# Kernel optimization log

Hardware: AMD Instinct MI355X
Metric: run time of the kernel (lower is better)

## Reference

```python
import jax, jax.numpy as jnp
import numpy as np

B, L, D, H = 2, 2048, 1024, 16
DK = D // H


def setup_inputs() -> dict:
    key = jax.random.key(0)
    ks = jax.random.split(key, 11)
    s = 1.0 / np.sqrt(D)
    inp = {
        "context_sequence": jax.random.normal(ks[0], (B, L, D), jnp.float32),
        "value_sequence": jax.random.normal(ks[1], (B, L, D), jnp.float32),
        "mask": jnp.tril(jnp.ones((L, L), jnp.int32)),  # causal mask [L, L]
        "Wq": jax.random.normal(ks[2], (D, D), jnp.float32) * s,
        "bq": jax.random.normal(ks[3], (D,), jnp.float32) * s,
        "Wk": jax.random.normal(ks[4], (D, D), jnp.float32) * s,
        "bk": jax.random.normal(ks[5], (D,), jnp.float32) * s,
        "Wv": jax.random.normal(ks[6], (D, D), jnp.float32) * s,
        "bv": jax.random.normal(ks[7], (D,), jnp.float32) * s,
        "Wo": jax.random.normal(ks[8], (D, D), jnp.float32) * s,
        "bo": jax.random.normal(ks[9], (D,), jnp.float32) * s,
    }
    return inp


def reference(context_sequence, value_sequence, mask, Wq, bq, Wk, bk, Wv, bv, Wo, bo):
    orig_dtype = context_sequence.dtype
    # QKV projections; Q,K from context, V from value stream
    Q = (context_sequence @ Wq + bq).reshape(B, L, H, DK)
    K = (context_sequence @ Wk + bk).reshape(B, L, H, DK)
    V = (value_sequence @ Wv + bv).reshape(B, L, H, DK)
    # fp32 QK^T with 1/sqrt(d_k) scaling -> [B, H, L, L]
    scores = jnp.einsum("bqhd,bkhd->bhqk", Q.astype(jnp.float32), K.astype(jnp.float32)) / jnp.sqrt(
        jnp.asarray(DK, jnp.float32)
    )
    # dtype-dependent neg fill (fp32 -> -inf); causal rows always have >=1 valid entry
    neg_fill = jnp.asarray(-jnp.inf, jnp.float32)
    scores = jnp.where(mask[None, None, :, :] == 0, neg_fill, scores)
    scores = scores.astype(orig_dtype)
    attn = jax.nn.softmax(scores, axis=-1)
    # dropout is identity in eval mode
    out = jnp.einsum("bhqk,bkhd->bqhd", attn, V).reshape(B, L, D)
    return out @ Wo + bo
```

## Files before the change

### kernel.cpp

```cpp
#include <hip/hip_runtime.h>
#include <hip/hip_bf16.h>
#include <stdint.h>

#define B_   2
#define L_   2048
#define D_   1024
#define H_   16
#define DK_  64

typedef __attribute__((ext_vector_type(4))) float f32x4;
typedef __attribute__((ext_vector_type(8))) short short8;
typedef unsigned short ushort_t;

__device__ __forceinline__ ushort_t f2bf(float f) {
    union { float f; uint32_t u; } v; v.f = f;
    uint32_t r = v.u + 0x7FFFu + ((v.u >> 16) & 1u);
    return (ushort_t)(r >> 16);
}
__device__ __forceinline__ float bf2f(ushort_t u) {
    union { uint32_t u; float f; } v; v.u = (uint32_t)u << 16; return v.f;
}

__device__ __forceinline__ void async_copy16(void* lds, const void* g) {
    __builtin_amdgcn_global_load_lds(
        (const __attribute__((address_space(1))) uint32_t*)g,
        (__attribute__((address_space(3))) uint32_t*)lds, 16, 0, 0);
}

__global__ void cast_f32_bf16(const float* __restrict__ s0, const float* __restrict__ s1,
                              ushort_t* __restrict__ d0, ushort_t* __restrict__ d1) {
    const float* s = blockIdx.z ? s1 : s0;
    ushort_t*    d = blockIdx.z ? d1 : d0;
    int i = (blockIdx.x * 256 + threadIdx.x) * 4;
    float4 v = *(const float4*)(s + i);
    ushort4 o;
    o.x = f2bf(v.x); o.y = f2bf(v.y); o.z = f2bf(v.z); o.w = f2bf(v.w);
    *(ushort4*)(d + i) = o;
}

__global__ void transpose_w(const float* __restrict__ w0, const float* __restrict__ w1,
                            const float* __restrict__ w2, const float* __restrict__ w3,
                            ushort_t* __restrict__ out) {
    __shared__ float tile[32][33];
    const float* w = (blockIdx.z == 0) ? w0 : (blockIdx.z == 1) ? w1 : (blockIdx.z == 2) ? w2 : w3;
    ushort_t* o = out + (size_t)blockIdx.z * D_ * D_;
    int tx = threadIdx.x, ty = threadIdx.y;
    int k0 = blockIdx.y * 32, d0 = blockIdx.x * 32;
#pragma unroll
    for (int i = 0; i < 4; i++)
        tile[ty + i * 8][tx] = w[(size_t)(k0 + ty + i * 8) * D_ + d0 + tx];
    __syncthreads();
#pragma unroll
    for (int i = 0; i < 4; i++)
        o[(size_t)(d0 + ty + i * 8) * D_ + k0 + tx] = f2bf(tile[tx][ty + i * 8]);
}

__device__ __forceinline__ void gemm_main(const ushort_t* __restrict__ A,
                                          const ushort_t* __restrict__ WT,
                                          char* smem, int m0, int n0, int tid,
                                          f32x4 (&acc)[4][4]) {
    const int wid = tid >> 6, lane = tid & 63;
    const int wm = (wid >> 1) * 64, wn = (wid & 1) * 64;
#pragma unroll
    for (int i = 0; i < 4; i++)
#pragma unroll
        for (int j = 0; j < 4; j++) { f32x4 z = {0.f, 0.f, 0.f, 0.f}; acc[i][j] = z; }

    auto stage = [&](int buf, int k0) {
        char* bA = smem + buf * 32768;
        char* bB = bA + 16384;
#pragma unroll
        for (int i = 0; i < 4; i++) {
            int flat = i * 256 + tid; int row = flat >> 3; int win = (flat & 7) * 16;
            const char* srcA = (const char*)A + ((size_t)(m0 + row) * D_ + k0) * 2 + (win ^ ((row & 7) << 4));
            async_copy16(bA + (i * 256 + wid * 64) * 16, srcA);
            const char* srcB = (const char*)WT + ((size_t)(n0 + row) * D_ + k0) * 2 + (win ^ ((row & 7) << 4));
            async_copy16(bB + (i * 256 + wid * 64) * 16, srcB);
        }
    };

    stage(0, 0);
    int cur = 0;
    for (int k0 = 0; k0 < D_; k0 += 64) {
        __syncthreads();
        if (k0 + 64 < D_) stage(cur ^ 1, k0 + 64);
        const char* bA = smem + cur * 32768;
        const char* bB = bA + 16384;
#pragma unroll
        for (int ks = 0; ks < 2; ks++) {
            short8 af[4], bf[4];
            int kb = ks * 64 + ((lane >> 4) << 4);
#pragma unroll
            for (int t = 0; t < 4; t++) {
                int ml = wm + t * 16 + (lane & 15);
                af[t] = *(const short8*)(bA + ml * 128 + (kb ^ ((ml & 7) << 4)));
                int nl = wn + t * 16 + (lane & 15);
                bf[t] = *(const short8*)(bB + nl * 128 + (kb ^ ((nl & 7) << 4)));
            }
#pragma unroll
            for (int mt = 0; mt < 4; mt++)
#pragma unroll
                for (int nt = 0; nt < 4; nt++)
                    acc[mt][nt] = __builtin_amdgcn_mfma_f32_16x16x32_bf16(af[mt], bf[nt], acc[mt][nt], 0, 0, 0);
        }
        cur ^= 1;
    }
}

#define QSCALE 0.18033688f

__global__ __launch_bounds__(256, 2) void gemm_qkv(
    const ushort_t* __restrict__ Xc, const ushort_t* __restrict__ Xv,
    const ushort_t* __restrict__ WT0,
    const float* __restrict__ bq, const float* __restrict__ bk, const float* __restrict__ bv,
    ushort_t* __restrict__ qw, ushort_t* __restrict__ kw, ushort_t* __restrict__ vtw) {
    __shared__ __align__(16) char smem[65536];
    const int z = blockIdx.z;
    const ushort_t* A  = (z == 2) ? Xv : Xc;
    const ushort_t* WT = WT0 + (size_t)z * D_ * D_;
    const float* bias  = (z == 0) ? bq : (z == 1) ? bk : bv;
    const int tid = threadIdx.x, wid = tid >> 6, lane = tid & 63;
    const int m0 = blockIdx.y * 128, n0 = blockIdx.x * 128;
    const int wm = (wid >> 1) * 64, wn = (wid & 1) * 64;
    f32x4 acc[4][4];
    gemm_main(A, WT, smem, m0, n0, tid, acc);
#pragma unroll
    for (int mt = 0; mt < 4; mt++)
#pragma unroll
        for (int nt = 0; nt < 4; nt++)
#pragma unroll
            for (int r = 0; r < 4; r++) {
                int m = m0 + wm + mt * 16 + ((lane >> 4) << 2) + r;
                int n = n0 + wn + nt * 16 + (lane & 15);
                float v = acc[mt][nt][r] + bias[n];
                int b = m >> 11, tok = m & 2047, h = n >> 6, dk = n & 63;
                if (z == 0)      qw[((size_t)(b * H_ + h) * L_ + tok) * DK_ + dk] = f2bf(v * QSCALE);
                else if (z == 1) kw[((size_t)(b * H_ + h) * L_ + tok) * DK_ + dk] = f2bf(v);
                else             vtw[((size_t)(b * H_ + h) * DK_ + dk) * L_ + tok] = f2bf(v);
            }
}

__global__ __launch_bounds__(256, 2) void gemm_out(
    const ushort_t* __restrict__ O, const ushort_t* __restrict__ WT,
    const float* __restrict__ bo, float* __restrict__ out) {
    __shared__ __align__(16) char smem[65536];
    const int tid = threadIdx.x, wid = tid >> 6, lane = tid & 63;
    const int m0 = blockIdx.y * 128, n0 = blockIdx.x * 128;
    const int wm = (wid >> 1) * 64, wn = (wid & 1) * 64;
    f32x4 acc[4][4];
    gemm_main(O, WT, smem, m0, n0, tid, acc);
#pragma unroll
    for (int mt = 0; mt < 4; mt++)
#pragma unroll
        for (int nt = 0; nt < 4; nt++)
#pragma unroll
            for (int r = 0; r < 4; r++) {
                int m = m0 + wm + mt * 16 + ((lane >> 4) << 2) + r;
                int n = n0 + wn + nt * 16 + (lane & 15);
                out[(size_t)m * D_ + n] = acc[mt][nt][r] + bo[n];
            }
}

__global__ __launch_bounds__(256, 2) void attn_kernel(
    const ushort_t* __restrict__ qws, const ushort_t* __restrict__ kws,
    const ushort_t* __restrict__ vtws, ushort_t* __restrict__ ows) {
    __shared__ __align__(16) char smem[37888];
    const int tid = threadIdx.x, wid = tid >> 6, lane = tid & 63;
    const int lo = lane & 15, hi = lane >> 4;
    const int bid = blockIdx.x;
    const int bh  = (bid & 7) * 4 + (bid >> 8);
    const int qtb = 31 - ((bid >> 3) & 31);
    const int Q0 = qtb * 64;
    char*  Pw = smem + wid * 9216;
    float* lw = (float*)(smem + 36864) + wid * 64;
    const int swz = (lo & 7) << 4;

    short8 ones;
#pragma unroll
    for (int i = 0; i < 8; i++) ones[i] = (short)0x3F80;
    const f32x4 minit = {-32.f, -32.f, -32.f, -32.f};

    short8 qf[4][2];
#pragma unroll
    for (int qt = 0; qt < 4; qt++)
#pragma unroll
        for (int ks = 0; ks < 2; ks++)
            qf[qt][ks] = *(const short8*)(qws + (size_t)(bh * L_ + Q0 + qt * 16 + lo) * DK_ + ks * 32 + hi * 8);

    f32x4 oa[4][4];
    f32x4 lf4[4];
#pragma unroll
    for (int qt = 0; qt < 4; qt++) {
        f32x4 z = {0.f, 0.f, 0.f, 0.f};
        lf4[qt] = z;
#pragma unroll
        for (int ot = 0; ot < 4; ot++) oa[qt][ot] = z;
    }

    const int ntiles = qtb + 1;
#pragma unroll 1
    for (int t = wid; t < ntiles; t += 4) {
        const int k0 = t * 64;
        const bool diag = (t == qtb);
        short8 vf[4][2];
#pragma unroll
        for (int ot = 0; ot < 4; ot++)
#pragma unroll
            for (int ks = 0; ks < 2; ks++)
                vf[ot][ks] = *(const short8*)(vtws + (size_t)(bh * DK_ + ot * 16 + lo) * L_ + k0 + ks * 32 + hi * 8);

#pragma unroll
        for (int kt = 0; kt < 4; kt++) {
            const ushort_t* krow = kws + (size_t)(bh * L_ + k0 + kt * 16 + lo) * DK_ + hi * 8;
            short8 kf0 = *(const short8*)(krow);
            short8 kf1 = *(const short8*)(krow + 32);
            const int kb = kt * 16 + 4 * hi;
#pragma unroll
            for (int qt = 0; qt < 4; qt++) {
                f32x4 s = __builtin_amdgcn_mfma_f32_16x16x32_bf16(kf0, qf[qt][0], minit, 0, 0, 0);
                s = __builtin_amdgcn_mfma_f32_16x16x32_bf16(kf1, qf[qt][1], s, 0, 0, 0);
                float p0 = exp2f(s[0]);
                float p1 = exp2f(s[1]);
                float p2 = exp2f(s[2]);
                float p3 = exp2f(s[3]);
                if (diag) {
                    const int qg = qt * 16 + lo;
                    p0 = (kb > qg)     ? 0.f : p0;
                    p1 = (kb + 1 > qg) ? 0.f : p1;
                    p2 = (kb + 2 > qg) ? 0.f : p2;
                    p3 = (kb + 3 > qg) ? 0.f : p3;
                }
                uint2 w;
                w.x = __builtin_amdgcn_perm(__float_as_uint(p1), __float_as_uint(p0), 0x07060302u);
                w.y = __builtin_amdgcn_perm(__float_as_uint(p3), __float_as_uint(p2), 0x07060302u);
                *(uint2*)(Pw + qt * 2048 + lo * 128 + ((kt * 32 + hi * 8) ^ swz)) = w;
            }
        }
#pragma unroll
        for (int qt = 0; qt < 4; qt++)
#pragma unroll
            for (int ks = 0; ks < 2; ks++) {
                short8 pf = *(const short8*)(Pw + qt * 2048 + lo * 128 + ((ks * 64 + hi * 16) ^ swz));
                lf4[qt] = __builtin_amdgcn_mfma_f32_16x16x32_bf16(pf, ones, lf4[qt], 0, 0, 0);
#pragma unroll
                for (int ot = 0; ot < 4; ot++)
                    oa[qt][ot] = __builtin_amdgcn_mfma_f32_16x16x32_bf16(pf, vf[ot][ks], oa[qt][ot], 0, 0, 0);
            }
    }

#pragma unroll
    for (int qt = 0; qt < 4; qt++)
#pragma unroll
        for (int ot = 0; ot < 4; ot++)
#pragma unroll
            for (int r = 0; r < 4; r++)
                *(ushort_t*)(Pw + (qt * 16 + 4 * hi + r) * 144 + (ot * 16 + lo) * 2) = f2bf(oa[qt][ot][r]);
    if (lo == 0) {
#pragma unroll
        for (int qt = 0; qt < 4; qt++)
            *(f32x4*)(lw + qt * 16 + 4 * hi) = lf4[qt];
    }
    __syncthreads();

    {
        const int q = tid >> 2, c = tid & 3;
        float acc[16];
#pragma unroll
        for (int j = 0; j < 16; j++) acc[j] = 0.f;
#pragma unroll
        for (int w = 0; w < 4; w++) {
            const char* base = smem + w * 9216 + q * 144 + c * 32;
            short8 a = *(const short8*)(base);
            short8 b = *(const short8*)(base + 16);
#pragma unroll
            for (int j = 0; j < 8; j++) acc[j]     += bf2f((ushort_t)a[j]);
#pragma unroll
            for (int j = 0; j < 8; j++) acc[8 + j] += bf2f((ushort_t)b[j]);
        }
        float ls = 0.f;
#pragma unroll
        for (int w = 0; w < 4; w++) ls += ((const float*)(smem + 36864))[w * 64 + q];
        float ri = 1.0f / ls;
        short8 o0, o1;
#pragma unroll
        for (int j = 0; j < 8; j++) o0[j] = (short)f2bf(acc[j] * ri);
#pragma unroll
        for (int j = 0; j < 8; j++) o1[j] = (short)f2bf(acc[8 + j] * ri);
        size_t ob = (size_t)((bh >> 4) * L_ + Q0 + q) * D_ + (bh & 15) * DK_ + c * 16;
        *(short8*)(ows + ob)     = o0;
        *(short8*)(ows + ob + 8) = o1;
    }
}

extern "C" void kernel_launch(void* const* d_in, const int* in_sizes, int n_in,
                              void* d_out, int out_size, void* d_ws, size_t ws_size,
                              hipStream_t stream) {
    (void)in_sizes; (void)n_in; (void)out_size; (void)ws_size;
    const float* ctx = (const float*)d_in[0];
    const float* val = (const float*)d_in[1];
    const float* Wq = (const float*)d_in[3];
    const float* bq = (const float*)d_in[4];
    const float* Wk = (const float*)d_in[5];
    const float* bk = (const float*)d_in[6];
    const float* Wv = (const float*)d_in[7];
    const float* bv = (const float*)d_in[8];
    const float* Wo = (const float*)d_in[9];
    const float* bo = (const float*)d_in[10];
    float* out = (float*)d_out;

    char* ws = (char*)d_ws;
    ushort_t* xc  = (ushort_t*)(ws);
    ushort_t* xv  = (ushort_t*)(ws + 8388608);
    ushort_t* wt  = (ushort_t*)(ws + 16777216);
    ushort_t* qws = (ushort_t*)(ws + 25165824);
    ushort_t* kws = (ushort_t*)(ws + 33554432);
    ushort_t* vtw = (ushort_t*)(ws + 41943040);

    cast_f32_bf16<<<dim3(4096, 1, 2), 256, 0, stream>>>(ctx, val, xc, xv);
    transpose_w<<<dim3(32, 32, 4), dim3(32, 8), 0, stream>>>(Wq, Wk, Wv, Wo, wt);
    gemm_qkv<<<dim3(8, 32, 3), 256, 0, stream>>>(xc, xv, wt, bq, bk, bv, qws, kws, vtw);
    attn_kernel<<<dim3(1024), 256, 0, stream>>>(qws, kws, vtw, xc );
    gemm_out<<<dim3(8, 32), 256, 0, stream>>>(xc, wt + (size_t)3 * D_ * D_, bo, out);
}
```

Measured before the change: 136.7 us.

## Split attention blocks into paired 32-row query tiles for causal load balance

Each attention block now handles two 32-row query tiles, j and 63-j, one after the other instead of a single 64-row tile, so every block does roughly the same amount of causal work. Per-wave register and LDS footprint shrink (fewer Q/O accumulators, a smaller P buffer), and launch bounds rise to 3 blocks per SM to raise occupancy. The cost is an extra reduction/sync pass per block and K/V tiles that are re-read for the two halves with less reuse per load.

```diff
diff --git a/kernel.cpp b/kernel.cpp
--- a/kernel.cpp
+++ b/kernel.cpp
@@ -161,18 +161,18 @@
             }
 }
 
-__global__ __launch_bounds__(256, 2) void attn_kernel(
+__global__ __launch_bounds__(256, 3) void attn_kernel(
     const ushort_t* __restrict__ qws, const ushort_t* __restrict__ kws,
     const ushort_t* __restrict__ vtws, ushort_t* __restrict__ ows) {
-    __shared__ __align__(16) char smem[37888];
+    __shared__ __align__(16) char smem[20992];
     const int tid = threadIdx.x, wid = tid >> 6, lane = tid & 63;
     const int lo = lane & 15, hi = lane >> 4;
     const int bid = blockIdx.x;
     const int bh  = (bid & 7) * 4 + (bid >> 8);
-    const int qtb = 31 - ((bid >> 3) & 31);
-    const int Q0 = qtb * 64;
-    char*  Pw = smem + wid * 9216;
-    float* lw = (float*)(smem + 36864) + wid * 64;
+    const int pi  = (bid >> 3) & 31;
+    char*  Pw = smem + wid * 5120;
+    float* lall = (float*)(smem + 20480);
+    float* lw = lall + wid * 32;
     const int swz = (lo & 7) << 4;
 
     short8 ones;
@@ -180,115 +180,115 @@
     for (int i = 0; i < 8; i++) ones[i] = (short)0x3F80;
     const f32x4 minit = {-32.f, -32.f, -32.f, -32.f};
 
-    short8 qf[4][2];
-#pragma unroll
-    for (int qt = 0; qt < 4; qt++)
-#pragma unroll
-        for (int ks = 0; ks < 2; ks++)
-            qf[qt][ks] = *(const short8*)(qws + (size_t)(bh * L_ + Q0 + qt * 16 + lo) * DK_ + ks * 32 + hi * 8);
-
-    f32x4 oa[4][4];
-    f32x4 lf4[4];
-#pragma unroll
-    for (int qt = 0; qt < 4; qt++) {
-        f32x4 z = {0.f, 0.f, 0.f, 0.f};
-        lf4[qt] = z;
-#pragma unroll
-        for (int ot = 0; ot < 4; ot++) oa[qt][ot] = z;
-    }
-
-    const int ntiles = qtb + 1;
 #pragma unroll 1
-    for (int t = wid; t < ntiles; t += 4) {
-        const int k0 = t * 64;
-        const bool diag = (t == qtb);
-        short8 vf[4][2];
-#pragma unroll
-        for (int ot = 0; ot < 4; ot++)
+    for (int half = 0; half < 2; half++) {
+        const int j  = half ? (63 - pi) : pi;
+        const int Q0 = j * 32;
+        const int ntiles = (j >> 1) + 1;
+
+        short8 qf[2][2];
+#pragma unroll
+        for (int qt = 0; qt < 2; qt++)
 #pragma unroll
             for (int ks = 0; ks < 2; ks++)
-                vf[ot][ks] = *(const short8*)(vtws + (size_t)(bh * DK_ + ot * 16 + lo) * L_ + k0 + ks * 32 + hi * 8);
-
-#pragma unroll
-        for (int kt = 0; kt < 4; kt++) {
-            const ushort_t* krow = kws + (size_t)(bh * L_ + k0 + kt * 16 + lo) * DK_ + hi * 8;
-            short8 kf0 = *(const short8*)(krow);
-            short8 kf1 = *(const short8*)(krow + 32);
-            const int kb = kt * 16 + 4 * hi;
-#pragma unroll
-            for (int qt = 0; qt < 4; qt++) {
-                f32x4 s = __builtin_amdgcn_mfma_f32_16x16x32_bf16(kf0, qf[qt][0], minit, 0, 0, 0);
-                s = __builtin_amdgcn_mfma_f32_16x16x32_bf16(kf1, qf[qt][1], s, 0, 0, 0);
-                float p0 = exp2f(s[0]);
-                float p1 = exp2f(s[1]);
-                float p2 = exp2f(s[2]);
-                float p3 = exp2f(s[3]);
-                if (diag) {
-                    const int qg = qt * 16 + lo;
-                    p0 = (kb > qg)     ? 0.f : p0;
-                    p1 = (kb + 1 > qg) ? 0.f : p1;
-                    p2 = (kb + 2 > qg) ? 0.f : p2;
-                    p3 = (kb + 3 > qg) ? 0.f : p3;
+                qf[qt][ks] = *(const short8*)(qws + (size_t)(bh * L_ + Q0 + qt * 16 + lo) * DK_ + ks * 32 + hi * 8);
+
+        f32x4 oa[2][4];
+        f32x4 lf4[2];
+#pragma unroll
+        for (int qt = 0; qt < 2; qt++) {
+            f32x4 z = {0.f, 0.f, 0.f, 0.f};
+            lf4[qt] = z;
+#pragma unroll
+            for (int ot = 0; ot < 4; ot++) oa[qt][ot] = z;
+        }
+
+#pragma unroll 1
+        for (int t = wid; t < ntiles; t += 4) {
+            const int k0 = t * 64;
+            const bool last = (t == ntiles - 1);
+            short8 vf[4][2];
+#pragma unroll
+            for (int ot = 0; ot < 4; ot++)
+#pragma unroll
+                for (int ks = 0; ks < 2; ks++)
+                    vf[ot][ks] = *(const short8*)(vtws + (size_t)(bh * DK_ + ot * 16 + lo) * L_ + k0 + ks * 32 + hi * 8);
+
+#pragma unroll
+            for (int kt = 0; kt < 4; kt++) {
+                const ushort_t* krow = kws + (size_t)(bh * L_ + k0 + kt * 16 + lo) * DK_ + hi * 8;
+                short8 kf0 = *(const short8*)(krow);
+                short8 kf1 = *(const short8*)(krow + 32);
+                const int kg = k0 + kt * 16 + 4 * hi;
+#pragma unroll
+                for (int qt = 0; qt < 2; qt++) {
+                    f32x4 s = __builtin_amdgcn_mfma_f32_16x16x32_bf16(kf0, qf[qt][0], minit, 0, 0, 0);
+                    s = __builtin_amdgcn_mfma_f32_16x16x32_bf16(kf1, qf[qt][1], s, 0, 0, 0);
+                    float p0 = exp2f(s[0]);
+                    float p1 = exp2f(s[1]);
+                    float p2 = exp2f(s[2]);
+                    float p3 = exp2f(s[3]);
+                    if (last) {
+                        const int qg = Q0 + qt * 16 + lo;
+                        p0 = (kg > qg)     ? 0.f : p0;
+                        p1 = (kg + 1 > qg) ? 0.f : p1;
+                        p2 = (kg + 2 > qg) ? 0.f : p2;
+                        p3 = (kg + 3 > qg) ? 0.f : p3;
+                    }
+                    uint2 w;
+                    w.x = __builtin_amdgcn_perm(__float_as_uint(p1), __float_as_uint(p0), 0x07060302u);
+                    w.y = __builtin_amdgcn_perm(__float_as_uint(p3), __float_as_uint(p2), 0x07060302u);
+                    *(uint2*)(Pw + (qt * 16 + lo) * 160 + ((kt * 32 + hi * 8) ^ swz)) = w;
                 }
-                uint2 w;
-                w.x = __builtin_amdgcn_perm(__float_as_uint(p1), __float_as_uint(p0), 0x07060302u);
-                w.y = __builtin_amdgcn_perm(__float_as_uint(p3), __float_as_uint(p2), 0x07060302u);
-                *(uint2*)(Pw + qt * 2048 + lo * 128 + ((kt * 32 + hi * 8) ^ swz)) = w;
-            }
-        }
-#pragma unroll
-        for (int qt = 0; qt < 4; qt++)
-#pragma unroll
-            for (int ks = 0; ks < 2; ks++) {
-                short8 pf = *(const short8*)(Pw + qt * 2048 + lo * 128 + ((ks * 64 + hi * 16) ^ swz));
-                lf4[qt] = __builtin_amdgcn_mfma_f32_16x16x32_bf16(pf, ones, lf4[qt], 0, 0, 0);
-#pragma unroll
-                for (int ot = 0; ot < 4; ot++)
-                    oa[qt][ot] = __builtin_amdgcn_mfma_f32_16x16x32_bf16(pf, vf[ot][ks], oa[qt][ot], 0, 0, 0);
-            }
-    }
-
-#pragma unroll
-    for (int qt = 0; qt < 4; qt++)
-#pragma unroll
-        for (int ot = 0; ot < 4; ot++)
-#pragma unroll
-            for (int r = 0; r < 4; r++)
-                *(ushort_t*)(Pw + (qt * 16 + 4 * hi + r) * 144 + (ot * 16 + lo) * 2) = f2bf(oa[qt][ot][r]);
-    if (lo == 0) {
-#pragma unroll
-        for (int qt = 0; qt < 4; qt++)
-            *(f32x4*)(lw + qt * 16 + 4 * hi) = lf4[qt];
-    }
-    __syncthreads();
-
-    {
-        const int q = tid >> 2, c = tid & 3;
-        float acc[16];
-#pragma unroll
-        for (int j = 0; j < 16; j++) acc[j] = 0.f;
-#pragma unroll
-        for (int w = 0; w < 4; w++) {
-            const char* base = smem + w * 9216 + q * 144 + c * 32;
-            short8 a = *(const short8*)(base);
-            short8 b = *(const short8*)(base + 16);
-#pragma unroll
-            for (int j = 0; j < 8; j++) acc[j]     += bf2f((ushort_t)a[j]);
-#pragma unroll
-            for (int j = 0; j < 8; j++) acc[8 + j] += bf2f((ushort_t)b[j]);
-        }
-        float ls = 0.f;
-#pragma unroll
-        for (int w = 0; w < 4; w++) ls += ((const float*)(smem + 36864))[w * 64 + q];
-        float ri = 1.0f / ls;
-        short8 o0, o1;
-#pragma unroll
-        for (int j = 0; j < 8; j++) o0[j] = (short)f2bf(acc[j] * ri);
-#pragma unroll
-        for (int j = 0; j < 8; j++) o1[j] = (short)f2bf(acc[8 + j] * ri);
-        size_t ob = (size_t)((bh >> 4) * L_ + Q0 + q) * D_ + (bh & 15) * DK_ + c * 16;
-        *(short8*)(ows + ob)     = o0;
-        *(short8*)(ows + ob + 8) = o1;
+            }
+#pragma unroll
+            for (int qt = 0; qt < 2; qt++)
+#pragma unroll
+                for (int ks = 0; ks < 2; ks++) {
+                    short8 pf = *(const short8*)(Pw + (qt * 16 + lo) * 160 + ((ks * 64 + hi * 16) ^ swz));
+                    lf4[qt] = __builtin_amdgcn_mfma_f32_16x16x32_bf16(pf, ones, lf4[qt], 0, 0, 0);
+#pragma unroll
+                    for (int ot = 0; ot < 4; ot++)
+                        oa[qt][ot] = __builtin_amdgcn_mfma_f32_16x16x32_bf16(pf, vf[ot][ks], oa[qt][ot], 0, 0, 0);
+                }
+        }
+
+#pragma unroll
+        for (int qt = 0; qt < 2; qt++)
+#pragma unroll
+            for (int ot = 0; ot < 4; ot++)
+#pragma unroll
+                for (int r = 0; r < 4; r++)
+                    *(ushort_t*)(Pw + (qt * 16 + 4 * hi + r) * 160 + (ot * 16 + lo) * 2) = f2bf(oa[qt][ot][r]);
+        if (lo == 0) {
+#pragma unroll
+            for (int qt = 0; qt < 2; qt++)
+                *(f32x4*)(lw + qt * 16 + 4 * hi) = lf4[qt];
+        }
+        __syncthreads();
+
+        {
+            const int q = tid >> 3, c = tid & 7;
+            float acc[8];
+#pragma unroll
+            for (int e = 0; e < 8; e++) acc[e] = 0.f;
+#pragma unroll
+            for (int w = 0; w < 4; w++) {
+                short8 a = *(const short8*)(smem + w * 5120 + q * 160 + c * 16);
+#pragma unroll
+                for (int e = 0; e < 8; e++) acc[e] += bf2f((ushort_t)a[e]);
+            }
+            float ls = 0.f;
+#pragma unroll
+            for (int w = 0; w < 4; w++) ls += lall[w * 32 + q];
+            float ri = 1.0f / ls;
+            short8 o;
+#pragma unroll
+            for (int e = 0; e < 8; e++) o[e] = (short)f2bf(acc[e] * ri);
+            size_t ob = (size_t)((bh >> 4) * L_ + Q0 + q) * D_ + (bh & 15) * DK_ + c * 8;
+            *(short8*)(ows + ob) = o;
+        }
+        __syncthreads();
     }
 }
 
```

Result: slower. 160.8 us (+17.6%).

## Pair causal query tiles per attention block and vectorize GEMM epilogue stores

Applied to the files above, without the earlier changes.

The attention kernel now launches half as many blocks, and each block handles two query tiles (pi and 31-pi). This evens out causal work across blocks and removes the tail imbalance from the heavy late tiles. The GEMMs swap the MFMA operand order so each lane holds four contiguous output columns (or tokens for V transposed), which lets the epilogues write packed uint2 and float4 stores and read biases as vectors instead of doing scattered scalar stores. The QKV GEMM is split into three templated launches, adding launch overhead and removing the concurrency the single z-grid launch had.

```diff
diff --git a/kernel.cpp b/kernel.cpp
--- a/kernel.cpp
+++ b/kernel.cpp
@@ -19,6 +19,9 @@
 }
 __device__ __forceinline__ float bf2f(ushort_t u) {
     union { uint32_t u; float f; } v; v.u = (uint32_t)u << 16; return v.f;
+}
+__device__ __forceinline__ uint32_t pack_bf16_rne(float a, float b) {
+    return (uint32_t)f2bf(a) | ((uint32_t)f2bf(b) << 16);
 }
 
 __device__ __forceinline__ void async_copy16(void* lds, const void* g) {
@@ -55,6 +58,7 @@
         o[(size_t)(d0 + ty + i * 8) * D_ + k0 + tx] = f2bf(tile[tx][ty + i * 8]);
 }
 
+template <bool SWAP>
 __device__ __forceinline__ void gemm_main(const ushort_t* __restrict__ A,
                                           const ushort_t* __restrict__ WT,
                                           char* smem, int m0, int n0, int tid,
@@ -101,7 +105,9 @@
             for (int mt = 0; mt < 4; mt++)
 #pragma unroll
                 for (int nt = 0; nt < 4; nt++)
-                    acc[mt][nt] = __builtin_amdgcn_mfma_f32_16x16x32_bf16(af[mt], bf[nt], acc[mt][nt], 0, 0, 0);
+                    acc[mt][nt] = SWAP
+                        ? __builtin_amdgcn_mfma_f32_16x16x32_bf16(bf[nt], af[mt], acc[mt][nt], 0, 0, 0)
+                        : __builtin_amdgcn_mfma_f32_16x16x32_bf16(af[mt], bf[nt], acc[mt][nt], 0, 0, 0);
         }
         cur ^= 1;
     }
@@ -109,35 +115,51 @@
 
 #define QSCALE 0.18033688f
 
-__global__ __launch_bounds__(256, 2) void gemm_qkv(
-    const ushort_t* __restrict__ Xc, const ushort_t* __restrict__ Xv,
-    const ushort_t* __restrict__ WT0,
-    const float* __restrict__ bq, const float* __restrict__ bk, const float* __restrict__ bv,
-    ushort_t* __restrict__ qw, ushort_t* __restrict__ kw, ushort_t* __restrict__ vtw) {
+template <int Z>
+__global__ __launch_bounds__(256, 2) void gemm_qkv_t(
+    const ushort_t* __restrict__ A, const ushort_t* __restrict__ WT,
+    const float* __restrict__ bias, ushort_t* __restrict__ outp) {
     __shared__ __align__(16) char smem[65536];
-    const int z = blockIdx.z;
-    const ushort_t* A  = (z == 2) ? Xv : Xc;
-    const ushort_t* WT = WT0 + (size_t)z * D_ * D_;
-    const float* bias  = (z == 0) ? bq : (z == 1) ? bk : bv;
     const int tid = threadIdx.x, wid = tid >> 6, lane = tid & 63;
+    const int lo = lane & 15, hi = lane >> 4;
     const int m0 = blockIdx.y * 128, n0 = blockIdx.x * 128;
     const int wm = (wid >> 1) * 64, wn = (wid & 1) * 64;
     f32x4 acc[4][4];
-    gemm_main(A, WT, smem, m0, n0, tid, acc);
-#pragma unroll
-    for (int mt = 0; mt < 4; mt++)
-#pragma unroll
-        for (int nt = 0; nt < 4; nt++)
-#pragma unroll
-            for (int r = 0; r < 4; r++) {
-                int m = m0 + wm + mt * 16 + ((lane >> 4) << 2) + r;
-                int n = n0 + wn + nt * 16 + (lane & 15);
-                float v = acc[mt][nt][r] + bias[n];
-                int b = m >> 11, tok = m & 2047, h = n >> 6, dk = n & 63;
-                if (z == 0)      qw[((size_t)(b * H_ + h) * L_ + tok) * DK_ + dk] = f2bf(v * QSCALE);
-                else if (z == 1) kw[((size_t)(b * H_ + h) * L_ + tok) * DK_ + dk] = f2bf(v);
-                else             vtw[((size_t)(b * H_ + h) * DK_ + dk) * L_ + tok] = f2bf(v);
-            }
+    gemm_main<(Z != 2)>(A, WT, smem, m0, n0, tid, acc);
+    if (Z != 2) {
+#pragma unroll
+        for (int mt = 0; mt < 4; mt++)
+#pragma unroll
+            for (int nt = 0; nt < 4; nt++) {
+                int m  = m0 + wm + mt * 16 + lo;
+                int nb = n0 + wn + nt * 16 + 4 * hi;
+                float4 b4 = *(const float4*)(bias + nb);
+                float v0 = acc[mt][nt][0] + b4.x;
+                float v1 = acc[mt][nt][1] + b4.y;
+                float v2 = acc[mt][nt][2] + b4.z;
+                float v3 = acc[mt][nt][3] + b4.w;
+                if (Z == 0) { v0 *= QSCALE; v1 *= QSCALE; v2 *= QSCALE; v3 *= QSCALE; }
+                int b = m >> 11, tok = m & 2047, h = nb >> 6, dk = nb & 63;
+                uint2 w;
+                w.x = pack_bf16_rne(v0, v1);
+                w.y = pack_bf16_rne(v2, v3);
+                *(uint2*)(outp + ((size_t)(b * H_ + h) * L_ + tok) * DK_ + dk) = w;
+            }
+    } else {
+#pragma unroll
+        for (int mt = 0; mt < 4; mt++)
+#pragma unroll
+            for (int nt = 0; nt < 4; nt++) {
+                int n  = n0 + wn + nt * 16 + lo;
+                int mb = m0 + wm + mt * 16 + 4 * hi;
+                float bv_ = bias[n];
+                int b = mb >> 11, tok = mb & 2047, h = n >> 6, dk = n & 63;
+                uint2 w;
+                w.x = pack_bf16_rne(acc[mt][nt][0] + bv_, acc[mt][nt][1] + bv_);
+                w.y = pack_bf16_rne(acc[mt][nt][2] + bv_, acc[mt][nt][3] + bv_);
+                *(uint2*)(outp + ((size_t)(b * H_ + h) * DK_ + dk) * L_ + tok) = w;
+            }
+    }
 }
 
 __global__ __launch_bounds__(256, 2) void gemm_out(
@@ -145,20 +167,25 @@
     const float* __restrict__ bo, float* __restrict__ out) {
     __shared__ __align__(16) char smem[65536];
     const int tid = threadIdx.x, wid = tid >> 6, lane = tid & 63;
+    const int lo = lane & 15, hi = lane >> 4;
     const int m0 = blockIdx.y * 128, n0 = blockIdx.x * 128;
     const int wm = (wid >> 1) * 64, wn = (wid & 1) * 64;
     f32x4 acc[4][4];
-    gemm_main(O, WT, smem, m0, n0, tid, acc);
+    gemm_main<true>(O, WT, smem, m0, n0, tid, acc);
 #pragma unroll
     for (int mt = 0; mt < 4; mt++)
 #pragma unroll
-        for (int nt = 0; nt < 4; nt++)
-#pragma unroll
-            for (int r = 0; r < 4; r++) {
-                int m = m0 + wm + mt * 16 + ((lane >> 4) << 2) + r;
-                int n = n0 + wn + nt * 16 + (lane & 15);
-                out[(size_t)m * D_ + n] = acc[mt][nt][r] + bo[n];
-            }
+        for (int nt = 0; nt < 4; nt++) {
+            int m  = m0 + wm + mt * 16 + lo;
+            int nb = n0 + wn + nt * 16 + 4 * hi;
+            float4 b4 = *(const float4*)(bo + nb);
+            float4 o;
+            o.x = acc[mt][nt][0] + b4.x;
+            o.y = acc[mt][nt][1] + b4.y;
+            o.z = acc[mt][nt][2] + b4.z;
+            o.w = acc[mt][nt][3] + b4.w;
+            *(float4*)(out + (size_t)m * D_ + nb) = o;
+        }
 }
 
 __global__ __launch_bounds__(256, 2) void attn_kernel(
@@ -168,11 +195,12 @@
     const int tid = threadIdx.x, wid = tid >> 6, lane = tid & 63;
     const int lo = lane & 15, hi = lane >> 4;
     const int bid = blockIdx.x;
-    const int bh  = (bid & 7) * 4 + (bid >> 8);
-    const int qtb = 31 - ((bid >> 3) & 31);
-    const int Q0 = qtb * 64;
+    const int xcd = bid & 7, slot = bid >> 3;
+    const int bh = xcd * 4 + (slot >> 4);
+    const int pi = slot & 15;
     char*  Pw = smem + wid * 9216;
-    float* lw = (float*)(smem + 36864) + wid * 64;
+    float* lall = (float*)(smem + 36864);
+    float* lw = lall + wid * 64;
     const int swz = (lo & 7) << 4;
 
     short8 ones;
@@ -180,115 +208,122 @@
     for (int i = 0; i < 8; i++) ones[i] = (short)0x3F80;
     const f32x4 minit = {-32.f, -32.f, -32.f, -32.f};
 
-    short8 qf[4][2];
-#pragma unroll
-    for (int qt = 0; qt < 4; qt++)
-#pragma unroll
-        for (int ks = 0; ks < 2; ks++)
-            qf[qt][ks] = *(const short8*)(qws + (size_t)(bh * L_ + Q0 + qt * 16 + lo) * DK_ + ks * 32 + hi * 8);
-
-    f32x4 oa[4][4];
-    f32x4 lf4[4];
-#pragma unroll
-    for (int qt = 0; qt < 4; qt++) {
-        f32x4 z = {0.f, 0.f, 0.f, 0.f};
-        lf4[qt] = z;
-#pragma unroll
-        for (int ot = 0; ot < 4; ot++) oa[qt][ot] = z;
-    }
-
-    const int ntiles = qtb + 1;
 #pragma unroll 1
-    for (int t = wid; t < ntiles; t += 4) {
-        const int k0 = t * 64;
-        const bool diag = (t == qtb);
-        short8 vf[4][2];
-#pragma unroll
-        for (int ot = 0; ot < 4; ot++)
+    for (int half = 0; half < 2; half++) {
+        const int qtb = half ? (31 - pi) : pi;
+        const int Q0 = qtb * 64;
+
+        short8 qf[4][2];
+#pragma unroll
+        for (int qt = 0; qt < 4; qt++)
 #pragma unroll
             for (int ks = 0; ks < 2; ks++)
-                vf[ot][ks] = *(const short8*)(vtws + (size_t)(bh * DK_ + ot * 16 + lo) * L_ + k0 + ks * 32 + hi * 8);
-
-#pragma unroll
-        for (int kt = 0; kt < 4; kt++) {
-            const ushort_t* krow = kws + (size_t)(bh * L_ + k0 + kt * 16 + lo) * DK_ + hi * 8;
-            short8 kf0 = *(const short8*)(krow);
-            short8 kf1 = *(const short8*)(krow + 32);
-            const int kb = kt * 16 + 4 * hi;
-#pragma unroll
-            for (int qt = 0; qt < 4; qt++) {
-                f32x4 s = __builtin_amdgcn_mfma_f32_16x16x32_bf16(kf0, qf[qt][0], minit, 0, 0, 0);
-                s = __builtin_amdgcn_mfma_f32_16x16x32_bf16(kf1, qf[qt][1], s, 0, 0, 0);
-                float p0 = exp2f(s[0]);
-                float p1 = exp2f(s[1]);
-                float p2 = exp2f(s[2]);
-                float p3 = exp2f(s[3]);
-                if (diag) {
-                    const int qg = qt * 16 + lo;
-                    p0 = (kb > qg)     ? 0.f : p0;
-                    p1 = (kb + 1 > qg) ? 0.f : p1;
-                    p2 = (kb + 2 > qg) ? 0.f : p2;
-                    p3 = (kb + 3 > qg) ? 0.f : p3;
+                qf[qt][ks] = *(const short8*)(qws + (size_t)(bh * L_ + Q0 + qt * 16 + lo) * DK_ + ks * 32 + hi * 8);
+
+        f32x4 oa[4][4];
+        f32x4 lf4[4];
+#pragma unroll
+        for (int qt = 0; qt < 4; qt++) {
+            f32x4 z = {0.f, 0.f, 0.f, 0.f};
+            lf4[qt] = z;
+#pragma unroll
+            for (int ot = 0; ot < 4; ot++) oa[qt][ot] = z;
+        }
+
+        const int ntiles = qtb + 1;
+#pragma unroll 1
+        for (int t = wid; t < ntiles; t += 4) {
+            const int k0 = t * 64;
+            const bool diag = (t == qtb);
+            short8 vf[4][2];
+#pragma unroll
+            for (int ot = 0; ot < 4; ot++)
+#pragma unroll
+                for (int ks = 0; ks < 2; ks++)
+                    vf[ot][ks] = *(const short8*)(vtws + (size_t)(bh * DK_ + ot * 16 + lo) * L_ + k0 + ks * 32 + hi * 8);
+
+#pragma unroll
+            for (int kt = 0; kt < 4; kt++) {
+                const ushort_t* krow = kws + (size_t)(bh * L_ + k0 + kt * 16 + lo) * DK_ + hi * 8;
+                short8 kf0 = *(const short8*)(krow);
+                short8 kf1 = *(const short8*)(krow + 32);
+                const int kb = kt * 16 + 4 * hi;
+#pragma unroll
+                for (int qt = 0; qt < 4; qt++) {
+                    f32x4 s = __builtin_amdgcn_mfma_f32_16x16x32_bf16(kf0, qf[qt][0], minit, 0, 0, 0);
+                    s = __builtin_amdgcn_mfma_f32_16x16x32_bf16(kf1, qf[qt][1], s, 0, 0, 0);
+                    float p0 = exp2f(s[0]);
+                    float p1 = exp2f(s[1]);
+                    float p2 = exp2f(s[2]);
+                    float p3 = exp2f(s[3]);
+                    if (diag) {
+                        const int qg = qt * 16 + lo;
+                        p0 = (kb > qg)     ? 0.f : p0;
+                        p1 = (kb + 1 > qg) ? 0.f : p1;
+                        p2 = (kb + 2 > qg) ? 0.f : p2;
+                        p3 = (kb + 3 > qg) ? 0.f : p3;
+                    }
+                    uint2 w;
+                    w.x = __builtin_amdgcn_perm(__float_as_uint(p1), __float_as_uint(p0), 0x07060302u);
+                    w.y = __builtin_amdgcn_perm(__float_as_uint(p3), __float_as_uint(p2), 0x07060302u);
+                    *(uint2*)(Pw + qt * 2048 + lo * 128 + ((kt * 32 + hi * 8) ^ swz)) = w;
                 }
-                uint2 w;
-                w.x = __builtin_amdgcn_perm(__float_as_uint(p1), __float_as_uint(p0), 0x07060302u);
-                w.y = __builtin_amdgcn_perm(__float_as_uint(p3), __float_as_uint(p2), 0x07060302u);
-                *(uint2*)(Pw + qt * 2048 + lo * 128 + ((kt * 32 + hi * 8) ^ swz)) = w;
-            }
-        }
+            }
+#pragma unroll
+            for (int qt = 0; qt < 4; qt++)
+#pragma unroll
+                for (int ks = 0; ks < 2; ks++) {
+                    short8 pf = *(const short8*)(Pw + qt * 2048 + lo * 128 + ((ks * 64 + hi * 16) ^ swz));
+                    lf4[qt] = __builtin_amdgcn_mfma_f32_16x16x32_bf16(pf, ones, lf4[qt], 0, 0, 0);
+#pragma unroll
+                    for (int ot = 0; ot < 4; ot++)
+                        oa[qt][ot] = __builtin_amdgcn_mfma_f32_16x16x32_bf16(pf, vf[ot][ks], oa[qt][ot], 0, 0, 0);
+                }
+        }
+
 #pragma unroll
         for (int qt = 0; qt < 4; qt++)
 #pragma unroll
-            for (int ks = 0; ks < 2; ks++) {
-                short8 pf = *(const short8*)(Pw + qt * 2048 + lo * 128 + ((ks * 64 + hi * 16) ^ swz));
-                lf4[qt] = __builtin_amdgcn_mfma_f32_16x16x32_bf16(pf, ones, lf4[qt], 0, 0, 0);
-#pragma unroll
-                for (int ot = 0; ot < 4; ot++)
-                    oa[qt][ot] = __builtin_amdgcn_mfma_f32_16x16x32_bf16(pf, vf[ot][ks], oa[qt][ot], 0, 0, 0);
-            }
-    }
-
-#pragma unroll
-    for (int qt = 0; qt < 4; qt++)
-#pragma unroll
-        for (int ot = 0; ot < 4; ot++)
-#pragma unroll
-            for (int r = 0; r < 4; r++)
-                *(ushort_t*)(Pw + (qt * 16 + 4 * hi + r) * 144 + (ot * 16 + lo) * 2) = f2bf(oa[qt][ot][r]);
-    if (lo == 0) {
-#pragma unroll
-        for (int qt = 0; qt < 4; qt++)
-            *(f32x4*)(lw + qt * 16 + 4 * hi) = lf4[qt];
-    }
-    __syncthreads();
-
-    {
-        const int q = tid >> 2, c = tid & 3;
-        float acc[16];
-#pragma unroll
-        for (int j = 0; j < 16; j++) acc[j] = 0.f;
-#pragma unroll
-        for (int w = 0; w < 4; w++) {
-            const char* base = smem + w * 9216 + q * 144 + c * 32;
-            short8 a = *(const short8*)(base);
-            short8 b = *(const short8*)(base + 16);
-#pragma unroll
-            for (int j = 0; j < 8; j++) acc[j]     += bf2f((ushort_t)a[j]);
-#pragma unroll
-            for (int j = 0; j < 8; j++) acc[8 + j] += bf2f((ushort_t)b[j]);
-        }
-        float ls = 0.f;
-#pragma unroll
-        for (int w = 0; w < 4; w++) ls += ((const float*)(smem + 36864))[w * 64 + q];
-        float ri = 1.0f / ls;
-        short8 o0, o1;
-#pragma unroll
-        for (int j = 0; j < 8; j++) o0[j] = (short)f2bf(acc[j] * ri);
-#pragma unroll
-        for (int j = 0; j < 8; j++) o1[j] = (short)f2bf(acc[8 + j] * ri);
-        size_t ob = (size_t)((bh >> 4) * L_ + Q0 + q) * D_ + (bh & 15) * DK_ + c * 16;
-        *(short8*)(ows + ob)     = o0;
-        *(short8*)(ows + ob + 8) = o1;
+            for (int ot = 0; ot < 4; ot++)
+#pragma unroll
+                for (int r = 0; r < 4; r++)
+                    *(ushort_t*)(Pw + (qt * 16 + 4 * hi + r) * 144 + (ot * 16 + lo) * 2) = f2bf(oa[qt][ot][r]);
+        if (lo == 0) {
+#pragma unroll
+            for (int qt = 0; qt < 4; qt++)
+                *(f32x4*)(lw + qt * 16 + 4 * hi) = lf4[qt];
+        }
+        __syncthreads();
+
+        {
+            const int q = tid >> 2, c = tid & 3;
+            float acc[16];
+#pragma unroll
+            for (int j = 0; j < 16; j++) acc[j] = 0.f;
+#pragma unroll
+            for (int w = 0; w < 4; w++) {
+                const char* base = smem + w * 9216 + q * 144 + c * 32;
+                short8 a = *(const short8*)(base);
+                short8 b = *(const short8*)(base + 16);
+#pragma unroll
+                for (int j = 0; j < 8; j++) acc[j]     += bf2f((ushort_t)a[j]);
+#pragma unroll
+                for (int j = 0; j < 8; j++) acc[8 + j] += bf2f((ushort_t)b[j]);
+            }
+            float ls = 0.f;
+#pragma unroll
+            for (int w = 0; w < 4; w++) ls += lall[w * 64 + q];
+            float ri = 1.0f / ls;
+            short8 o0, o1;
+#pragma unroll
+            for (int j = 0; j < 8; j++) o0[j] = (short)f2bf(acc[j] * ri);
+#pragma unroll
+            for (int j = 0; j < 8; j++) o1[j] = (short)f2bf(acc[8 + j] * ri);
+            size_t ob = (size_t)((bh >> 4) * L_ + Q0 + q) * D_ + (bh & 15) * DK_ + c * 16;
+            *(short8*)(ows + ob)     = o0;
+            *(short8*)(ows + ob + 8) = o1;
+        }
+        __syncthreads();
     }
 }
 
@@ -318,7 +353,9 @@
 
     cast_f32_bf16<<<dim3(4096, 1, 2), 256, 0, stream>>>(ctx, val, xc, xv);
     transpose_w<<<dim3(32, 32, 4), dim3(32, 8), 0, stream>>>(Wq, Wk, Wv, Wo, wt);
-    gemm_qkv<<<dim3(8, 32, 3), 256, 0, stream>>>(xc, xv, wt, bq, bk, bv, qws, kws, vtw);
-    attn_kernel<<<dim3(1024), 256, 0, stream>>>(qws, kws, vtw, xc );
+    gemm_qkv_t<0><<<dim3(8, 32), 256, 0, stream>>>(xc, wt,                       bq, qws);
+    gemm_qkv_t<1><<<dim3(8, 32), 256, 0, stream>>>(xc, wt + (size_t)1 * D_ * D_, bk, kws);
+    gemm_qkv_t<2><<<dim3(8, 32), 256, 0, stream>>>(xv, wt + (size_t)2 * D_ * D_, bv, vtw);
+    attn_kernel<<<dim3(512), 256, 0, stream>>>(qws, kws, vtw, xc );
     gemm_out<<<dim3(8, 32), 256, 0, stream>>>(xc, wt + (size_t)3 * D_ * D_, bo, out);
 }
```

Result: faster. 126.8 us (-7.3%).
